# Optimization experiments

Measured on AMD Instinct MI355X. Metric: run time of the kernel, lower is better.

The kernel has to match this reference:

```python
import jax, jax.numpy as jnp
import numpy as np

B, S, HID = 2, 2048, 2048
NH, NKV, DH = 32, 8, 64
WIN = 1024


def rotate_half(x):
    x1, x2 = x[..., : x.shape[-1] // 2], x[..., x.shape[-1] // 2:]
    return jnp.concatenate((-x2, x1), axis=-1)


def setup_inputs() -> dict:
    key = jax.random.key(0)
    ks = jax.random.split(key, 8)
    hidden_states = jax.random.normal(ks[0], (B, S, HID), dtype=jnp.float32)
    # real RoPE tables: [B, S, DH]
    inv_freq = 1.0 / (10000.0 ** (np.arange(0, DH, 2, dtype=np.float32) / DH))
    ang = np.arange(S, dtype=np.float32)[:, None] * inv_freq[None, :]  # [S, DH/2]
    emb = np.concatenate([ang, ang], axis=-1)  # [S, DH]
    cos = jnp.broadcast_to(jnp.asarray(np.cos(emb)), (B, S, DH))
    sin = jnp.broadcast_to(jnp.asarray(np.sin(emb)), (B, S, DH))
    sc = 0.02
    Wq = jax.random.normal(ks[1], (NH * DH, HID), dtype=jnp.float32) * sc
    Wk = jax.random.normal(ks[2], (NKV * DH, HID), dtype=jnp.float32) * sc
    Wv = jax.random.normal(ks[3], (NKV * DH, HID), dtype=jnp.float32) * sc
    Wo = jax.random.normal(ks[4], (HID, NH * DH), dtype=jnp.float32) * sc
    return {"hidden_states": hidden_states, "cos": cos, "sin": sin,
            "Wq": Wq, "Wk": Wk, "Wv": Wv, "Wo": Wo}


def sliding_window_mask(q_len, k_len, dtype):
    half = WIN // 2
    qi = jnp.arange(q_len)[:, None]
    ki = jnp.arange(k_len)[None, :]
    last = jnp.clip(qi + half, None, k_len - 1)
    first = jnp.clip(qi - half, 0, None)
    visible = (ki >= first) & (ki <= last)
    minv = jnp.finfo(dtype).min
    return jnp.where(visible, jnp.array(0.0, dtype), jnp.array(minv, dtype))  # [q_len, k_len]


def reference(hidden_states, cos, sin, Wq, Wk, Wv, Wo):
    b, s, _ = hidden_states.shape
    scale = DH ** -0.5
    q = (hidden_states @ Wq.T).reshape(b, s, NH, DH).transpose(0, 2, 1, 3)   # [B,NH,S,DH]
    k = (hidden_states @ Wk.T).reshape(b, s, NKV, DH).transpose(0, 2, 1, 3)  # [B,NKV,S,DH]
    v = (hidden_states @ Wv.T).reshape(b, s, NKV, DH).transpose(0, 2, 1, 3)
    c, sn = cos[:, None, :, :], sin[:, None, :, :]  # broadcast over heads
    q = q * c + rotate_half(q) * sn
    k = k * c + rotate_half(k) * sn
    groups = NH // NKV
    k = jnp.repeat(k, groups, axis=1)  # [B,NH,S,DH]
    v = jnp.repeat(v, groups, axis=1)
    mask = sliding_window_mask(s, s, hidden_states.dtype)  # [S,S]
    scores = jnp.einsum("bhqd,bhkd->bhqk", q, k) * scale + mask  # dense quadratic bias add
    attn = jax.nn.softmax(scores, axis=-1)
    out = jnp.einsum("bhqk,bhkd->bhqd", attn, v)
    out = out.transpose(0, 2, 1, 3).reshape(b, s, NH * DH)
    return out @ Wo.T
```

## Files before the change

### kernel.cpp

```cpp
#include <hip/hip_runtime.h>
#include <hip/hip_bf16.h>
#include <stdint.h>
#include <stddef.h>

#define S_LEN 2048
#define HIDDEN 2048
#define NHEAD 32
#define NKVH 8
#define DHEAD 64
#define BATCH 2
#define HALFW 512
#define QSCALE 0.18033688011112042f

typedef __attribute__((ext_vector_type(4))) float f32x4;
typedef __attribute__((ext_vector_type(8))) short short8;
typedef __attribute__((ext_vector_type(4))) short short4v;
typedef __attribute__((ext_vector_type(2))) unsigned int u32x2;

__device__ __forceinline__ unsigned short f2bf(float f) {
  unsigned u = __builtin_bit_cast(unsigned, f);
  u += 0x7fffu + ((u >> 16) & 1u);
  return (unsigned short)(u >> 16);
}
__device__ __forceinline__ float bf2f(unsigned short h) {
  unsigned u = ((unsigned)h) << 16;
  return __builtin_bit_cast(float, u);
}
__device__ __forceinline__ unsigned cvt_pk_bf16(float lo, float hi) {
  unsigned r;
  asm("v_cvt_pk_bf16_f32 %0, %1, %2" : "=v"(r) : "v"(lo), "v"(hi));
  return r;
}

__global__ void k_cvt5(const float* __restrict__ s0, const float* __restrict__ s1,
                       const float* __restrict__ s2, const float* __restrict__ s3,
                       const float* __restrict__ s4,
                       unsigned short* __restrict__ d0, unsigned short* __restrict__ d1,
                       unsigned short* __restrict__ d2, unsigned short* __restrict__ d3,
                       unsigned short* __restrict__ d4) {
  int i = blockIdx.x * blockDim.x + threadIdx.x;
#pragma unroll 1
  for (int it = 0; it < 9; ++it, i += 524288) {
    const float* src;
    unsigned short* dst;
    int base;
    if (i < 2097152)      { src = s0; dst = d0; base = 0; }
    else if (i < 3145728) { src = s1; dst = d1; base = 2097152; }
    else if (i < 3407872) { src = s2; dst = d2; base = 3145728; }
    else if (i < 3670016) { src = s3; dst = d3; base = 3407872; }
    else                  { src = s4; dst = d4; base = 3670016; }
    int j = i - base;
    float4 v = reinterpret_cast<const float4*>(src)[j];
    short4v o;
    o[0] = (short)f2bf(v.x);
    o[1] = (short)f2bf(v.y);
    o[2] = (short)f2bf(v.z);
    o[3] = (short)f2bf(v.w);
    reinterpret_cast<short4v*>(dst)[j] = o;
  }
}

template <int MODE>
__global__ __launch_bounds__(256) void k_gemm_bt(const unsigned short* __restrict__ A,
                                                 const unsigned short* __restrict__ Bw,
                                                 void* __restrict__ Cout,
                                                 const float* __restrict__ cosb,
                                                 const float* __restrict__ sinb,
                                                 unsigned short* __restrict__ Qr,
                                                 unsigned short* __restrict__ Kr,
                                                 unsigned short* __restrict__ Vrow,
                                                 int M, int N, int K) {
  __shared__ unsigned short As[128][32];
  __shared__ unsigned short Bs[128][32];
  const int tid = threadIdx.x;
  const int wid = tid >> 6;
  const int lane = tid & 63;
  const int l15 = lane & 15;
  const int lhi = lane >> 4;
  const int bm = blockIdx.y * 128;
  const int bn = blockIdx.x * 128;
  const int wm = (wid >> 1) * 64;
  const int wn = (wid & 1) * 64;
  f32x4 acc[4][4] = {};

  const int xq = (l15 >> 1) & 3;
  const int rc0 = (lhi ^ xq) * 16;

  for (int k0 = 0; k0 < K; k0 += 32) {
#pragma unroll
    for (int i = 0; i < 2; ++i) {
      int u = i * 256 + tid;
      int row = u >> 2, c8 = u & 3;
      int cs = c8 ^ ((row >> 1) & 3);
      const unsigned short* ga = A + (size_t)(bm + row) * K + k0 + cs * 8;
      const unsigned short* gb = Bw + (size_t)(bn + row) * K + k0 + cs * 8;
      __builtin_amdgcn_global_load_lds(
          (const __attribute__((address_space(1))) unsigned int*)(const void*)ga,
          (__attribute__((address_space(3))) unsigned int*)(void*)((char*)&As[0][0] + i * 4096 + wid * 1024),
          16, 0, 0);
      __builtin_amdgcn_global_load_lds(
          (const __attribute__((address_space(1))) unsigned int*)(const void*)gb,
          (__attribute__((address_space(3))) unsigned int*)(void*)((char*)&Bs[0][0] + i * 4096 + wid * 1024),
          16, 0, 0);
    }
    __syncthreads();

    short8 af[4], bfr[4];
#pragma unroll
    for (int m = 0; m < 4; ++m)
      af[m] = *reinterpret_cast<const short8*>(
          (const char*)&As[0][0] + (size_t)(wm + m * 16 + l15) * 64 + rc0);
#pragma unroll
    for (int n = 0; n < 4; ++n)
      bfr[n] = *reinterpret_cast<const short8*>(
          (const char*)&Bs[0][0] + (size_t)(wn + n * 16 + l15) * 64 + rc0);
#pragma unroll
    for (int m = 0; m < 4; ++m)
#pragma unroll
      for (int n = 0; n < 4; ++n)
        acc[m][n] = __builtin_amdgcn_mfma_f32_16x16x32_bf16(af[m], bfr[n], acc[m][n], 0, 0, 0);
    __syncthreads();
  }

  if (MODE == 1) {
#pragma unroll
    for (int m = 0; m < 4; ++m) {
#pragma unroll
      for (int r = 0; r < 4; ++r) {
        int row = bm + wm + m * 16 + lhi * 4 + r;
#pragma unroll
        for (int n = 0; n < 4; ++n) {
          int col = bn + wn + n * 16 + l15;
          ((float*)Cout)[(size_t)row * N + col] = acc[m][n][r];
        }
      }
    }
  } else {
    const int hc = (bn + wn) >> 6;
#pragma unroll
    for (int m = 0; m < 4; ++m) {
#pragma unroll
      for (int r = 0; r < 4; ++r) {
        int row = bm + wm + m * 16 + lhi * 4 + r;
        int b = row >> 11, s = row & 2047;
        if (hc < 40) {
#pragma unroll
          for (int n = 0; n < 2; ++n) {
            int d = n * 16 + l15;
            float c = cosb[(size_t)row * DHEAD + d];
            float sn = sinb[(size_t)row * DHEAD + d];
            float x1 = acc[m][n][r];
            float x2 = acc[m][n + 2][r];
            float o1 = x1 * c - x2 * sn;
            float o2 = x2 * c + x1 * sn;
            if (hc < 32) {
              size_t o = ((size_t)(b * NHEAD + hc) * S_LEN + s) * DHEAD + d;
              Qr[o] = f2bf(o1 * QSCALE);
              Qr[o + 32] = f2bf(o2 * QSCALE);
            } else {
              size_t o = ((size_t)(b * NKVH + (hc - 32)) * S_LEN + s) * DHEAD + d;
              Kr[o] = f2bf(o1);
              Kr[o + 32] = f2bf(o2);
            }
          }
        } else {
#pragma unroll
          for (int n = 0; n < 4; ++n) {
            int d = n * 16 + l15;
            size_t o = ((size_t)(b * NKVH + (hc - 40)) * S_LEN + s) * DHEAD + d;
            Vrow[o] = f2bf(acc[m][n][r]);
          }
        }
      }
    }
  }
}

__global__ void k_vt(const unsigned short* __restrict__ Vrow, unsigned short* __restrict__ Vt) {
  __shared__ unsigned short t[64][68];
  int s0 = blockIdx.x * 64;
  int g = blockIdx.y;
  int tid = threadIdx.x;
#pragma unroll
  for (int it = 0; it < 4; ++it) {
    int u = it * 256 + tid;
    int srow = u >> 4, c4 = u & 15;
    short4v v = *reinterpret_cast<const short4v*>(
        &Vrow[((size_t)g * S_LEN + s0 + srow) * DHEAD + c4 * 4]);
    *reinterpret_cast<short4v*>(&t[srow][c4 * 4]) = v;
  }
  __syncthreads();
#pragma unroll
  for (int it = 0; it < 4; ++it) {
    int u = it * 256 + tid;
    int d = u >> 4, s4 = u & 15;
    short4v v;
#pragma unroll
    for (int j = 0; j < 4; ++j) v[j] = t[s4 * 4 + j][d];
    *reinterpret_cast<short4v*>(
        &Vt[((size_t)g * DHEAD + d) * S_LEN + s0 + s4 * 4]) = v;
  }
}

__global__ __launch_bounds__(256, 4) void k_attn(const unsigned short* __restrict__ Qr,
                                                 const unsigned short* __restrict__ Kr,
                                                 const unsigned short* __restrict__ Vt,
                                                 unsigned short* __restrict__ AO) {
  __shared__ unsigned short Ks[2][64][64];
  __shared__ unsigned short Vs[2][64][64];
  __shared__ unsigned short Pl[4][16][64];

  const int tid = threadIdx.x, w = tid >> 6, lane = tid & 63;
  const int l15 = lane & 15, lhi = lane >> 4;

  int p = blockIdx.x;
  int L = (p & 7) * 256 + (p >> 3);
  int g = L >> 7;
  int b = g >> 3, hk = g & 7;
  int r_ = L & 127;
  int h = hk * 4 + (r_ >> 5);
  int q0b = (r_ & 31) * 64;
  const int qw = q0b + w * 16;

  const unsigned short* Qh = Qr + (size_t)(b * NHEAD + h) * S_LEN * DHEAD;
  const unsigned short* Kh = Kr + (size_t)(b * NKVH + hk) * S_LEN * DHEAD;
  const unsigned short* Vh = Vt + (size_t)(b * NKVH + hk) * DHEAD * S_LEN;

  short8 qf[2];
#pragma unroll
  for (int c = 0; c < 2; ++c)
    qf[c] = *reinterpret_cast<const short8*>(&Qh[(size_t)(qw + l15) * DHEAD + c * 32 + lhi * 8]);

  f32x4 o[4] = {};
  float den = 0.f;
  const int q = qw + l15;
  const int kvisLo = q - HALFW, kvisHi = q + HALFW;

  char* plbase = (char*)&Pl[w][0][0];
  const int swzp = (l15 & 7) << 4;

  int klo = q0b - HALFW; if (klo < 0) klo = 0;
  klo &= ~63;
  int khi = q0b + 63 + HALFW; if (khi > S_LEN - 1) khi = S_LEN - 1;
  const int nt = ((khi + 1 - klo) + 63) >> 6;

  auto stage = [&](int bufidx, int kbb) {
#pragma unroll
    for (int i = 0; i < 2; ++i) {
      int u = i * 256 + tid;
      int row = u >> 3, c16 = u & 7;
      int sc = c16 ^ (row & 7);
      __builtin_amdgcn_global_load_lds(
          (const __attribute__((address_space(1))) unsigned int*)(const void*)
              (Kh + (size_t)(kbb + row) * DHEAD + sc * 8),
          (__attribute__((address_space(3))) unsigned int*)(void*)
              ((char*)&Ks[bufidx][0][0] + u * 16),
          16, 0, 0);
      __builtin_amdgcn_global_load_lds(
          (const __attribute__((address_space(1))) unsigned int*)(const void*)
              (Vh + (size_t)row * S_LEN + kbb + sc * 8),
          (__attribute__((address_space(3))) unsigned int*)(void*)
              ((char*)&Vs[bufidx][0][0] + u * 16),
          16, 0, 0);
    }
  };

  int cur = 0;
  stage(0, klo);
  __syncthreads();

  for (int t = 0; t < nt; ++t) {
    const int kb = klo + t * 64;
    if (t + 1 < nt) stage(cur ^ 1, kb + 64);

    f32x4 sacc[4] = {};
    __builtin_amdgcn_s_setprio(1);
#pragma unroll
    for (int hh = 0; hh < 4; ++hh) {
      int kr = hh * 16 + l15;
      const char* kbase = (const char*)&Ks[cur][0][0] + kr * 128;
      short8 kf0 = *reinterpret_cast<const short8*>(kbase + ((lhi ^ (kr & 7)) * 16));
      short8 kf1 = *reinterpret_cast<const short8*>(kbase + (((4 + lhi) ^ (kr & 7)) * 16));
      sacc[hh] = __builtin_amdgcn_mfma_f32_16x16x32_bf16(kf0, qf[0], sacc[hh], 0, 0, 0);
      sacc[hh] = __builtin_amdgcn_mfma_f32_16x16x32_bf16(kf1, qf[1], sacc[hh], 0, 0, 0);
    }
    __builtin_amdgcn_s_setprio(0);

    const bool inter = (kb >= qw + 15 - HALFW) && (kb + 63 <= qw + HALFW);
    if (inter) {
#pragma unroll
      for (int hh = 0; hh < 4; ++hh) {
        float p0 = __builtin_amdgcn_exp2f(sacc[hh][0]);
        float p1 = __builtin_amdgcn_exp2f(sacc[hh][1]);
        float p2 = __builtin_amdgcn_exp2f(sacc[hh][2]);
        float p3 = __builtin_amdgcn_exp2f(sacc[hh][3]);
        den += (p0 + p1) + (p2 + p3);
        u32x2 pw;
        pw[0] = cvt_pk_bf16(p0, p1);
        pw[1] = cvt_pk_bf16(p2, p3);
        *(u32x2*)(plbase + ((l15 * 128 + hh * 32 + lhi * 8) ^ swzp)) = pw;
      }
    } else {
#pragma unroll
      for (int hh = 0; hh < 4; ++hh) {
        float pp[4];
#pragma unroll
        for (int r = 0; r < 4; ++r) {
          int key = kb + hh * 16 + lhi * 4 + r;
          bool vis = (key >= kvisLo) && (key <= kvisHi);
          pp[r] = vis ? __builtin_amdgcn_exp2f(sacc[hh][r]) : 0.0f;
        }
        den += (pp[0] + pp[1]) + (pp[2] + pp[3]);
        u32x2 pw;
        pw[0] = cvt_pk_bf16(pp[0], pp[1]);
        pw[1] = cvt_pk_bf16(pp[2], pp[3]);
        *(u32x2*)(plbase + ((l15 * 128 + hh * 32 + lhi * 8) ^ swzp)) = pw;
      }
    }
    asm volatile("s_waitcnt lgkmcnt(0)" ::: "memory");
    __builtin_amdgcn_sched_barrier(0);

    short8 pf0 = *reinterpret_cast<const short8*>(plbase + ((l15 * 128 + lhi * 16) ^ swzp));
    short8 pf1 = *reinterpret_cast<const short8*>(plbase + ((l15 * 128 + 64 + lhi * 16) ^ swzp));
    __builtin_amdgcn_s_setprio(1);
#pragma unroll
    for (int c = 0; c < 4; ++c) {
      int d = c * 16 + l15;
      const char* vbase = (const char*)&Vs[cur][0][0] + d * 128;
      short8 vf0 = *reinterpret_cast<const short8*>(vbase + ((lhi ^ (d & 7)) * 16));
      short8 vf1 = *reinterpret_cast<const short8*>(vbase + (((4 + lhi) ^ (d & 7)) * 16));
      o[c] = __builtin_amdgcn_mfma_f32_16x16x32_bf16(pf0, vf0, o[c], 0, 0, 0);
      o[c] = __builtin_amdgcn_mfma_f32_16x16x32_bf16(pf1, vf1, o[c], 0, 0, 0);
    }
    __builtin_amdgcn_s_setprio(0);

    __syncthreads();
    cur ^= 1;
  }

  den += __shfl_xor(den, 16);
  den += __shfl_xor(den, 32);

#pragma unroll
  for (int r = 0; r < 4; ++r) {
    int qo = qw + lhi * 4 + r;
    float dr = __shfl(den, lhi * 4 + r, 64);
    float dinv = 1.0f / dr;
#pragma unroll
    for (int c = 0; c < 4; ++c)
      AO[(size_t)(b * S_LEN + qo) * HIDDEN + h * DHEAD + c * 16 + l15] = f2bf(o[c][r] * dinv);
  }
}

extern "C" void kernel_launch(void* const* d_in, const int* in_sizes, int n_in,
                              void* d_out, int out_size, void* d_ws, size_t ws_size,
                              hipStream_t stream) {
  const float* hs   = (const float*)d_in[0];
  const float* cosb = (const float*)d_in[1];
  const float* sinb = (const float*)d_in[2];
  const float* Wq   = (const float*)d_in[3];
  const float* Wk   = (const float*)d_in[4];
  const float* Wv   = (const float*)d_in[5];
  const float* Wo   = (const float*)d_in[6];

  char* ws = (char*)d_ws;
  unsigned short* Xbf  = (unsigned short*)(ws);
  unsigned short* Wqkv = (unsigned short*)(ws + 16777216);
  unsigned short* Vt   = (unsigned short*)(ws + 29360128);
  unsigned short* AO   = (unsigned short*)(ws + 33554432);
  unsigned short* Wob  = (unsigned short*)(ws + 54525952);

  unsigned short* Qr   = (unsigned short*)d_out;
  unsigned short* Kr   = Qr + (size_t)BATCH * NKVH * S_LEN * DHEAD * 4;
  unsigned short* Vrow = Kr + (size_t)BATCH * NKVH * S_LEN * DHEAD;

  k_cvt5<<<2048, 256, 0, stream>>>(hs, Wq, Wk, Wv, Wo,
                                   Xbf, Wqkv, Wqkv + 4194304, Wqkv + 5242880, Wob);

  k_gemm_bt<2><<<dim3(3072 / 128, 4096 / 128), 256, 0, stream>>>(
      Xbf, Wqkv, nullptr, cosb, sinb, Qr, Kr, Vrow, 4096, 3072, 2048);

  k_vt<<<dim3(S_LEN / 64, BATCH * NKVH), 256, 0, stream>>>(Vrow, Vt);

  k_attn<<<BATCH * NHEAD * (S_LEN / 64), 256, 0, stream>>>(Qr, Kr, Vt, AO);

  k_gemm_bt<1><<<dim3(2048 / 128, 4096 / 128), 256, 0, stream>>>(
      AO, Wob, d_out, nullptr, nullptr, nullptr, nullptr, nullptr, 4096, 2048, 2048);
}
```

Before: 213.9 us.

## Double K-step per barrier and remap GEMM tiles by XCD for L2 locality

The GEMM kernel now stages two 32-wide K slices into a doubled LDS buffer per iteration, which halves the number of barrier pairs per K sweep. It also replaces the 2D grid with a 1D grid and remaps block IDs so that each XCD (bid & 7) owns a contiguous band of N-columns, aiming for better L2 reuse of weight tiles. The cost is double the LDS footprint per block, which may reduce occupancy, and there is still no overlap between loads and MFMA within an iteration.

After: 214.9 us. Within noise of the previous version (+0.5%).

```diff
diff --git a/kernel.cpp b/kernel.cpp
--- a/kernel.cpp
+++ b/kernel.cpp
@@ -60,7 +60,7 @@
   }
 }
 
-template <int MODE>
+template <int MODE, int NTX>
 __global__ __launch_bounds__(256) void k_gemm_bt(const unsigned short* __restrict__ A,
                                                  const unsigned short* __restrict__ Bw,
                                                  void* __restrict__ Cout,
@@ -70,15 +70,23 @@
                                                  unsigned short* __restrict__ Kr,
                                                  unsigned short* __restrict__ Vrow,
                                                  int M, int N, int K) {
-  __shared__ unsigned short As[128][32];
-  __shared__ unsigned short Bs[128][32];
+  __shared__ unsigned short As[2][128][32];
+  __shared__ unsigned short Bs[2][128][32];
   const int tid = threadIdx.x;
   const int wid = tid >> 6;
   const int lane = tid & 63;
   const int l15 = lane & 15;
   const int lhi = lane >> 4;
-  const int bm = blockIdx.y * 128;
-  const int bn = blockIdx.x * 128;
+
+  const int nxcol = NTX >> 3;
+  const int bid = blockIdx.x;
+  const int xcd = bid & 7;
+  const int w2 = bid >> 3;
+  const int tx = xcd * nxcol + (w2 % nxcol);
+  const int ty = w2 / nxcol;
+  const int bm = ty * 128;
+  const int bn = tx * 128;
+
   const int wm = (wid >> 1) * 64;
   const int wn = (wid & 1) * 64;
   f32x4 acc[4][4] = {};
@@ -86,39 +94,47 @@
   const int xq = (l15 >> 1) & 3;
   const int rc0 = (lhi ^ xq) * 16;
 
-  for (int k0 = 0; k0 < K; k0 += 32) {
-#pragma unroll
-    for (int i = 0; i < 2; ++i) {
-      int u = i * 256 + tid;
-      int row = u >> 2, c8 = u & 3;
-      int cs = c8 ^ ((row >> 1) & 3);
-      const unsigned short* ga = A + (size_t)(bm + row) * K + k0 + cs * 8;
-      const unsigned short* gb = Bw + (size_t)(bn + row) * K + k0 + cs * 8;
-      __builtin_amdgcn_global_load_lds(
-          (const __attribute__((address_space(1))) unsigned int*)(const void*)ga,
-          (__attribute__((address_space(3))) unsigned int*)(void*)((char*)&As[0][0] + i * 4096 + wid * 1024),
-          16, 0, 0);
-      __builtin_amdgcn_global_load_lds(
-          (const __attribute__((address_space(1))) unsigned int*)(const void*)gb,
-          (__attribute__((address_space(3))) unsigned int*)(void*)((char*)&Bs[0][0] + i * 4096 + wid * 1024),
-          16, 0, 0);
+  for (int k0 = 0; k0 < K; k0 += 64) {
+#pragma unroll
+    for (int kk = 0; kk < 2; ++kk) {
+#pragma unroll
+      for (int i = 0; i < 2; ++i) {
+        int u = i * 256 + tid;
+        int row = u >> 2, c8 = u & 3;
+        int cs = c8 ^ ((row >> 1) & 3);
+        const unsigned short* ga = A + (size_t)(bm + row) * K + k0 + kk * 32 + cs * 8;
+        const unsigned short* gb = Bw + (size_t)(bn + row) * K + k0 + kk * 32 + cs * 8;
+        __builtin_amdgcn_global_load_lds(
+            (const __attribute__((address_space(1))) unsigned int*)(const void*)ga,
+            (__attribute__((address_space(3))) unsigned int*)(void*)
+                ((char*)&As[0][0][0] + kk * 8192 + i * 4096 + wid * 1024),
+            16, 0, 0);
+        __builtin_amdgcn_global_load_lds(
+            (const __attribute__((address_space(1))) unsigned int*)(const void*)gb,
+            (__attribute__((address_space(3))) unsigned int*)(void*)
+                ((char*)&Bs[0][0][0] + kk * 8192 + i * 4096 + wid * 1024),
+            16, 0, 0);
+      }
     }
     __syncthreads();
 
-    short8 af[4], bfr[4];
-#pragma unroll
-    for (int m = 0; m < 4; ++m)
-      af[m] = *reinterpret_cast<const short8*>(
-          (const char*)&As[0][0] + (size_t)(wm + m * 16 + l15) * 64 + rc0);
-#pragma unroll
-    for (int n = 0; n < 4; ++n)
-      bfr[n] = *reinterpret_cast<const short8*>(
-          (const char*)&Bs[0][0] + (size_t)(wn + n * 16 + l15) * 64 + rc0);
-#pragma unroll
-    for (int m = 0; m < 4; ++m)
+#pragma unroll
+    for (int kk = 0; kk < 2; ++kk) {
+      short8 af[4], bfr[4];
+#pragma unroll
+      for (int m = 0; m < 4; ++m)
+        af[m] = *reinterpret_cast<const short8*>(
+            (const char*)&As[0][0][0] + kk * 8192 + (size_t)(wm + m * 16 + l15) * 64 + rc0);
 #pragma unroll
       for (int n = 0; n < 4; ++n)
-        acc[m][n] = __builtin_amdgcn_mfma_f32_16x16x32_bf16(af[m], bfr[n], acc[m][n], 0, 0, 0);
+        bfr[n] = *reinterpret_cast<const short8*>(
+            (const char*)&Bs[0][0][0] + kk * 8192 + (size_t)(wn + n * 16 + l15) * 64 + rc0);
+#pragma unroll
+      for (int m = 0; m < 4; ++m)
+#pragma unroll
+        for (int n = 0; n < 4; ++n)
+          acc[m][n] = __builtin_amdgcn_mfma_f32_16x16x32_bf16(af[m], bfr[n], acc[m][n], 0, 0, 0);
+    }
     __syncthreads();
   }
 
@@ -377,13 +393,13 @@
   k_cvt5<<<2048, 256, 0, stream>>>(hs, Wq, Wk, Wv, Wo,
                                    Xbf, Wqkv, Wqkv + 4194304, Wqkv + 5242880, Wob);
 
-  k_gemm_bt<2><<<dim3(3072 / 128, 4096 / 128), 256, 0, stream>>>(
+  k_gemm_bt<2, 24><<<dim3(768), 256, 0, stream>>>(
       Xbf, Wqkv, nullptr, cosb, sinb, Qr, Kr, Vrow, 4096, 3072, 2048);
 
   k_vt<<<dim3(S_LEN / 64, BATCH * NKVH), 256, 0, stream>>>(Vrow, Vt);
 
   k_attn<<<BATCH * NHEAD * (S_LEN / 64), 256, 0, stream>>>(Qr, Kr, Vt, AO);
 
-  k_gemm_bt<1><<<dim3(2048 / 128, 4096 / 128), 256, 0, stream>>>(
+  k_gemm_bt<1, 16><<<dim3(512), 256, 0, stream>>>(
       AO, Wob, d_out, nullptr, nullptr, nullptr, nullptr, nullptr, 4096, 2048, 2048);
 }
```
